# Optimization experiments

Hardware: AMD Instinct MI355X
Metric: run time of the kernel (lower is better)

Reference implementation:

```python
import jax, jax.numpy as jnp
import numpy as np

N_LETTERS = 256
EMBED_DIM = 1024
HIDDEN_DIM = 2048
SEQ_LEN = 4096


def setup_inputs() -> dict:
    key = jax.random.key(0)
    ks = jax.random.split(key, 8)
    s_e = 1.0 / np.sqrt(EMBED_DIM)
    s_h = 1.0 / np.sqrt(HIDDEN_DIM)
    return {
        "input_ids": jax.random.randint(ks[0], (SEQ_LEN,), 0, N_LETTERS, dtype=jnp.int64)
        if jax.config.jax_enable_x64 else jax.random.randint(ks[0], (SEQ_LEN,), 0, N_LETTERS, dtype=jnp.int32),
        "h0": jnp.zeros((1, 1, HIDDEN_DIM), jnp.float32),
        "c0": jnp.zeros((1, 1, HIDDEN_DIM), jnp.float32),
        "W_emb": jax.random.normal(ks[1], (N_LETTERS, EMBED_DIM), jnp.float32),
        "W_ih": jax.random.normal(ks[2], (4 * HIDDEN_DIM, EMBED_DIM), jnp.float32) * s_e,
        "W_hh": jax.random.normal(ks[3], (4 * HIDDEN_DIM, HIDDEN_DIM), jnp.float32) * s_h,
        "b_ih": jnp.zeros((4 * HIDDEN_DIM,), jnp.float32),
        "b_hh": jnp.zeros((4 * HIDDEN_DIM,), jnp.float32),
        "W_out": jax.random.normal(ks[4], (N_LETTERS, HIDDEN_DIM), jnp.float32) * s_h,
        "b_out": jnp.zeros((N_LETTERS,), jnp.float32),
    }


def reference(input_ids, h0, c0, W_emb, W_ih, W_hh, b_ih, b_hh, W_out, b_out):
    H = W_hh.shape[1]
    emb = W_emb[input_ids]                       # [L, E]
    # Precompute the input-side gate projections for all timesteps (batched GEMM).
    x_gates = emb @ W_ih.T + (b_ih + b_hh)       # [L, 4H]

    def step(carry, xg):
        h, c = carry                             # [H], [H]
        gates = xg + W_hh @ h                    # [4H], PyTorch order i,f,g,o
        i = jax.nn.sigmoid(gates[0 * H:1 * H])
        f = jax.nn.sigmoid(gates[1 * H:2 * H])
        g = jnp.tanh(gates[2 * H:3 * H])
        o = jax.nn.sigmoid(gates[3 * H:4 * H])
        c_new = f * c + i * g
        h_new = o * jnp.tanh(c_new)
        return (h_new, c_new), h_new

    (hL, cL), hs = jax.lax.scan(step, (h0[0, 0], c0[0, 0]), x_gates)  # hs: [L, H]
    logits = hs @ W_out.T + b_out                # [L, n_letters]
    # Dropout(p=0.1) is identity in eval mode.
    out = jax.nn.log_softmax(jax.nn.relu(logits), axis=-1)
    return out, hL[None, None, :], cL[None, None, :]
```

## Files before the change

### kernel.cpp

```cpp
#include <hip/hip_runtime.h>
#include <hip/hip_bf16.h>

#define SEQ 4096
#define EMB 1024
#define HID 2048
#define G4  8192
#define NL  256

typedef __attribute__((ext_vector_type(8))) short bf16x8;
typedef __attribute__((ext_vector_type(4))) float f32x4;

static __device__ __forceinline__ unsigned short f2bf(float f) {
    unsigned int x = __builtin_bit_cast(unsigned int, f);
    return (unsigned short)((x + 0x7FFFu + ((x >> 16) & 1u)) >> 16);
}
static __device__ __forceinline__ float bf2f(unsigned short u) {
    return __builtin_bit_cast(float, ((unsigned int)u) << 16);
}
static __device__ __forceinline__ unsigned long long aload(const unsigned long long* p) {
    return __hip_atomic_load(p, __ATOMIC_RELAXED, __HIP_MEMORY_SCOPE_AGENT);
}
static __device__ __forceinline__ float frcp(float x) {
    return __builtin_amdgcn_rcpf(x);
}
static __device__ __forceinline__ float fsigm(float x) {
    return frcp(1.f + __expf(-x));
}
static __device__ __forceinline__ float ftanh(float x) {
    return 1.f - 2.f * frcp(__expf(2.f * x) + 1.f);
}

__global__ __launch_bounds__(256) void k_f2b(const float* __restrict__ in,
                                             unsigned short* __restrict__ out, int n) {
    int i = (blockIdx.x * 256 + threadIdx.x) * 4;
    if (i < n) {
        float4 v = *(const float4*)&in[i];
        ushort4 u;
        u.x = f2bf(v.x); u.y = f2bf(v.y); u.z = f2bf(v.z); u.w = f2bf(v.w);
        *(ushort4*)&out[i] = u;
    }
}

__global__ __launch_bounds__(256) void k_emb(const int* __restrict__ ids,
                                             const float* __restrict__ W_emb,
                                             unsigned short* __restrict__ out) {
    int t = blockIdx.x;
    int e0 = threadIdx.x * 4;
    const float4 v = *(const float4*)&W_emb[(size_t)ids[t] * EMB + e0];
    ushort4 u;
    u.x = f2bf(v.x); u.y = f2bf(v.y); u.z = f2bf(v.z); u.w = f2bf(v.w);
    *(ushort4*)&out[(size_t)t * EMB + e0] = u;
}

#define BM 128
#define BN 128
#define BK 32
__global__ __launch_bounds__(256) void k_gemm_bt(
    const unsigned short* __restrict__ A, const unsigned short* __restrict__ B,
    const float* __restrict__ bias1, const float* __restrict__ bias2,
    float* __restrict__ Cf, unsigned short* __restrict__ Cb,
    int M, int N, int K)
{
    __shared__ unsigned short As[BM * BK];
    __shared__ unsigned short Bs[BN * BK];
    const int bm = blockIdx.x * BM;
    const int bn = blockIdx.y * BN;
    const int tid = threadIdx.x;
    const int wave = tid >> 6, lane = tid & 63;
    const int wm = (wave & 1) * 64, wn = (wave >> 1) * 64;
    const int row16 = lane & 15, quad = lane >> 4;

    f32x4 acc[4][4];
#pragma unroll
    for (int i = 0; i < 4; ++i)
#pragma unroll
        for (int j = 0; j < 4; ++j) acc[i][j] = (f32x4){0.f, 0.f, 0.f, 0.f};

    for (int k0 = 0; k0 < K; k0 += BK) {
        __syncthreads();
#pragma unroll
        for (int s = 0; s < 2; ++s) {
            int c = tid + s * 256;
            int r = c >> 2, col = (c & 3) * 8;
            *(uint4*)&As[r * BK + col] = *(const uint4*)&A[(size_t)(bm + r) * K + k0 + col];
            *(uint4*)&Bs[r * BK + col] = *(const uint4*)&B[(size_t)(bn + r) * K + k0 + col];
        }
        __syncthreads();
        bf16x8 af[4], bfr[4];
#pragma unroll
        for (int i = 0; i < 4; ++i) {
            af[i]  = *(const bf16x8*)&As[(wm + i * 16 + row16) * BK + quad * 8];
            bfr[i] = *(const bf16x8*)&Bs[(wn + i * 16 + row16) * BK + quad * 8];
        }
#pragma unroll
        for (int i = 0; i < 4; ++i)
#pragma unroll
            for (int j = 0; j < 4; ++j)
                acc[i][j] = __builtin_amdgcn_mfma_f32_16x16x32_bf16(af[i], bfr[j], acc[i][j], 0, 0, 0);
    }

#pragma unroll
    for (int j = 0; j < 4; ++j) {
        int col = bn + wn + j * 16 + row16;
        float bsum = (bias1 ? bias1[col] : 0.f) + (bias2 ? bias2[col] : 0.f);
#pragma unroll
        for (int i = 0; i < 4; ++i) {
#pragma unroll
            for (int r = 0; r < 4; ++r) {
                int row = bm + wm + i * 16 + quad * 4 + r;
                float v = acc[i][j][r] + bsum;
                if (Cf) Cf[(size_t)row * N + col] = v;
                else    Cb[(size_t)row * N + ((col & 2047) << 2) + (col >> 11)] = f2bf(v);
            }
        }
    }
}

#define LSTM_LDS 90112
__global__ __launch_bounds__(1024, 1) void k_lstm(
    const unsigned short* __restrict__ Whhb,
    const unsigned short* __restrict__ xg,
    const float* __restrict__ h0, const float* __restrict__ c0,
    unsigned short* __restrict__ hsb,
    float* __restrict__ outHC,
    unsigned long long* __restrict__ hcomm)
{
    extern __shared__ char smem[];
    float* LDSp = (float*)smem;

    const int b = blockIdx.x, tid = threadIdx.x;
    const int wave = tid >> 6, lane = tid & 63;
    const int sub = lane & 15, quad = lane >> 4;

    const int qa = (sub >> 3), qb = 2 + (sub >> 3), j = sub & 7;
    const unsigned short* wa = Whhb + ((size_t)(qa * HID + b * 8 + j)) * HID + wave * 128 + quad * 8;
    const unsigned short* wb = Whhb + ((size_t)(qb * HID + b * 8 + j)) * HID + wave * 128 + quad * 8;
    bf16x8 afrA[4], afrB[4];
#pragma unroll
    for (int c = 0; c < 4; ++c) {
        afrA[c] = *(const bf16x8*)(wa + c * 32);
        afrB[c] = *(const bf16x8*)(wb + c * 32);
    }

    float creg = 0.f;
    if (tid < 8) creg = c0[b * 8 + tid];

    for (int t = 0; t < SEQ; ++t) {
        float xq0 = 0.f, xq1 = 0.f, xq2 = 0.f, xq3 = 0.f;
        if (wave == 0 && lane < 8) {
            uint2 w2 = *(const uint2*)(xg + (size_t)t * G4 + (size_t)(b * 8 + lane) * 4);
            xq0 = bf2f((unsigned short)(w2.x & 0xffff));
            xq1 = bf2f((unsigned short)(w2.x >> 16));
            xq2 = bf2f((unsigned short)(w2.y & 0xffff));
            xq3 = bf2f((unsigned short)(w2.y >> 16));
        }

        f32x4 accA0 = (f32x4){0.f, 0.f, 0.f, 0.f};
        f32x4 accA1 = (f32x4){0.f, 0.f, 0.f, 0.f};
        f32x4 accB0 = (f32x4){0.f, 0.f, 0.f, 0.f};
        f32x4 accB1 = (f32x4){0.f, 0.f, 0.f, 0.f};

        if (t == 0) {
#pragma unroll
            for (int c = 0; c < 4; ++c) {
                const float* hp = h0 + wave * 128 + c * 32 + quad * 8;
                float4 va = *(const float4*)hp;
                float4 vb = *(const float4*)(hp + 4);
                uint4 d;
                d.x = (unsigned)f2bf(va.x) | ((unsigned)f2bf(va.y) << 16);
                d.y = (unsigned)f2bf(va.z) | ((unsigned)f2bf(va.w) << 16);
                d.z = (unsigned)f2bf(vb.x) | ((unsigned)f2bf(vb.y) << 16);
                d.w = (unsigned)f2bf(vb.z) | ((unsigned)f2bf(vb.w) << 16);
                bf16x8 hf = __builtin_bit_cast(bf16x8, d);
                if (c < 2) {
                    accA0 = __builtin_amdgcn_mfma_f32_16x16x32_bf16(afrA[c], hf, accA0, 0, 0, 0);
                    accB0 = __builtin_amdgcn_mfma_f32_16x16x32_bf16(afrB[c], hf, accB0, 0, 0, 0);
                } else {
                    accA1 = __builtin_amdgcn_mfma_f32_16x16x32_bf16(afrA[c], hf, accA1, 0, 0, 0);
                    accB1 = __builtin_amdgcn_mfma_f32_16x16x32_bf16(afrB[c], hf, accB1, 0, 0, 0);
                }
            }
        } else {
            const unsigned long long* sp =
                hcomm + (size_t)((t - 1) & 1) * 16384 + (size_t)(b & 7) * 2048
                      + (size_t)(wave * 16 + (lane >> 2)) * 8 + (lane & 3);
            const unsigned tag = (unsigned)t;
            unsigned long long x = aload(sp);
            if ((unsigned)(x >> 32) != tag) {
                __builtin_amdgcn_s_sleep(8);
                for (;;) {
                    unsigned long long x1 = aload(sp);
                    unsigned long long x2 = aload(sp);
                    if ((unsigned)(x1 >> 32) == tag) { x = x1; break; }
                    if ((unsigned)(x2 >> 32) == tag) { x = x2; break; }
                    __builtin_amdgcn_s_sleep(1);
                }
            }
            int myd = (int)(unsigned)x;
#pragma unroll
            for (int c = 0; c < 4; ++c) {
                const int sl = c * 16 + quad * 4;
                uint4 d;
                d.x = (unsigned)__shfl(myd, sl + 0);
                d.y = (unsigned)__shfl(myd, sl + 1);
                d.z = (unsigned)__shfl(myd, sl + 2);
                d.w = (unsigned)__shfl(myd, sl + 3);
                bf16x8 hf = __builtin_bit_cast(bf16x8, d);
                if (c < 2) {
                    accA0 = __builtin_amdgcn_mfma_f32_16x16x32_bf16(afrA[c], hf, accA0, 0, 0, 0);
                    accB0 = __builtin_amdgcn_mfma_f32_16x16x32_bf16(afrB[c], hf, accB0, 0, 0, 0);
                } else {
                    accA1 = __builtin_amdgcn_mfma_f32_16x16x32_bf16(afrA[c], hf, accA1, 0, 0, 0);
                    accB1 = __builtin_amdgcn_mfma_f32_16x16x32_bf16(afrB[c], hf, accB1, 0, 0, 0);
                }
            }
        }
        f32x4 acc0 = accA0 + accA1;
        f32x4 acc1 = accB0 + accB1;

        float* P = LDSp + (t & 1) * 640;
        if (sub == 0) {
#pragma unroll
            for (int r = 0; r < 4; ++r) {
                P[(quad * 4 + r) * 20 + wave]      = acc0[r];
                P[(16 + quad * 4 + r) * 20 + wave] = acc1[r];
            }
        }
        __syncthreads();

        if (wave == 0) {
            __builtin_amdgcn_s_setprio(1);
            float g = 0.f;
            if (lane < 32) {
                const float* rp = P + lane * 20;
                f32x4 s = *(const f32x4*)rp;
                s += *(const f32x4*)(rp + 4);
                s += *(const f32x4*)(rp + 8);
                s += *(const f32x4*)(rp + 12);
                g = s[0] + s[1] + s[2] + s[3];
            }
            float gF = __shfl(g, 8 + lane);
            float gG = __shfl(g, 16 + lane);
            float gO = __shfl(g, 24 + lane);
            unsigned hv = 0;
            float cn = 0.f, hn = 0.f;
            if (lane < 8) {
                float gi = g  + xq0;
                float gf = gF + xq1;
                float gg = gG + xq2;
                float go = gO + xq3;
                float i_ = fsigm(gi);
                float f_ = fsigm(gf);
                float g_ = ftanh(gg);
                float o_ = fsigm(go);
                cn = f_ * creg + i_ * g_;
                hn = o_ * ftanh(cn);
                creg = cn;
                hv = (unsigned)f2bf(hn);
            }
            {
                int jj = lane & 3;
                unsigned lo = (unsigned)__shfl((int)hv, 2 * jj);
                unsigned hi = (unsigned)__shfl((int)hv, 2 * jj + 1);
                if (lane < 32) {
                    unsigned long long wrd =
                        (((unsigned long long)(unsigned)(t + 1)) << 32)
                        | (unsigned long long)(lo | (hi << 16));
                    __hip_atomic_store(
                        &hcomm[(size_t)(t & 1) * 16384 + (size_t)(lane >> 2) * 2048 + b * 8 + jj],
                        wrd, __ATOMIC_RELAXED, __HIP_MEMORY_SCOPE_AGENT);
                }
            }
            __builtin_amdgcn_s_setprio(0);
            if (lane < 8) {
                hsb[(size_t)t * HID + b * 8 + lane] = (unsigned short)hv;
                if (t == SEQ - 1) {
                    outHC[b * 8 + lane] = hn;
                    outHC[HID + b * 8 + lane] = cn;
                }
            }
        }
    }
}

__global__ __launch_bounds__(256) void k_softmax(const float* __restrict__ logits,
                                                 float* __restrict__ out) {
    int row = blockIdx.x * 4 + (threadIdx.x >> 6);
    int lane = threadIdx.x & 63;
    const float* Lr = logits + (size_t)row * NL;
    float4 v = *(const float4*)&Lr[lane * 4];
    v.x = fmaxf(v.x, 0.f); v.y = fmaxf(v.y, 0.f);
    v.z = fmaxf(v.z, 0.f); v.w = fmaxf(v.w, 0.f);
    float m = fmaxf(fmaxf(v.x, v.y), fmaxf(v.z, v.w));
#pragma unroll
    for (int off = 32; off > 0; off >>= 1) m = fmaxf(m, __shfl_xor(m, off));
    float e = __expf(v.x - m) + __expf(v.y - m) + __expf(v.z - m) + __expf(v.w - m);
#pragma unroll
    for (int off = 32; off > 0; off >>= 1) e += __shfl_xor(e, off);
    float ls = __logf(e) + m;
    float4 o;
    o.x = v.x - ls; o.y = v.y - ls; o.z = v.z - ls; o.w = v.w - ls;
    *(float4*)&out[(size_t)row * NL + lane * 4] = o;
}

extern "C" void kernel_launch(void* const* d_in, const int* in_sizes, int n_in,
                              void* d_out, int out_size, void* d_ws, size_t ws_size,
                              hipStream_t stream) {
    const int*   ids   = (const int*)d_in[0];
    const float* h0    = (const float*)d_in[1];
    const float* c0    = (const float*)d_in[2];
    const float* W_emb = (const float*)d_in[3];
    const float* W_ih  = (const float*)d_in[4];
    const float* W_hh  = (const float*)d_in[5];
    const float* b_ih  = (const float*)d_in[6];
    const float* b_hh  = (const float*)d_in[7];
    const float* W_out = (const float*)d_in[8];
    const float* b_out = (const float*)d_in[9];
    float* out = (float*)d_out;

    char* ws = (char*)d_ws;
    unsigned short* xg    = (unsigned short*)(ws);
    unsigned short* hsb   = (unsigned short*)(ws + 67108864);
    unsigned short* Wihb  = (unsigned short*)(ws + 83886080);
    unsigned short* embb  = (unsigned short*)(ws + 100663296);
    unsigned short* Woutb = (unsigned short*)(ws + 109051904);
    float*          logit = (float*)(ws + 110100480);
    unsigned short* Whhb  = (unsigned short*)(ws + 114294784);
    unsigned long long* hcomm = (unsigned long long*)(ws + 147849216);

    k_f2b<<<(G4 * EMB / 4 + 255) / 256, 256, 0, stream>>>(W_ih, Wihb, G4 * EMB);
    k_f2b<<<(NL * HID / 4 + 255) / 256, 256, 0, stream>>>(W_out, Woutb, NL * HID);
    k_f2b<<<(G4 * HID / 4 + 255) / 256, 256, 0, stream>>>(W_hh, Whhb, G4 * HID);
    k_emb<<<SEQ, 256, 0, stream>>>(ids, W_emb, embb);

    dim3 g1(SEQ / BM, G4 / BN);
    k_gemm_bt<<<g1, 256, 0, stream>>>(embb, Wihb, b_ih, b_hh, nullptr, xg, SEQ, G4, EMB);

    hipFuncSetAttribute((const void*)k_lstm, hipFuncAttributeMaxDynamicSharedMemorySize, LSTM_LDS);
    k_lstm<<<256, 1024, LSTM_LDS, stream>>>(Whhb, xg, h0, c0, hsb, out + (size_t)SEQ * NL, hcomm);

    dim3 g2(SEQ / BM, NL / BN);
    k_gemm_bt<<<g2, 256, 0, stream>>>(hsb, Woutb, b_out, nullptr, logit, nullptr, SEQ, NL, HID);

    k_softmax<<<SEQ / 4, 256, 0, stream>>>(logit, out);
}
```

Measured before the change: 9.659 ms.

## Spread LSTM gate reduction and cell update across four waves

The per-step LDS reduction of the 16 wave partials and the gate nonlinearities, previously done serially by wave 0, are now split across four waves. Each wave handles two hidden units, using 64 lanes with a butterfly shuffle reduction. Each wave publishes its own packed h word to the cross-block communication buffer. The aim is to shorten the serial critical path of each recurrent step. The cost is more waves taking part in the tail of every step and more store instructions issued to hcomm.

Result: slower. 13.23 ms (+37.0%).

```diff
diff --git a/kernel.cpp b/kernel.cpp
--- a/kernel.cpp
+++ b/kernel.cpp
@@ -143,12 +143,13 @@
     }
 
     float creg = 0.f;
-    if (tid < 8) creg = c0[b * 8 + tid];
+    if (wave < 4 && (lane & 55) == 0) creg = c0[b * 8 + wave * 2 + (lane >> 3)];
 
     for (int t = 0; t < SEQ; ++t) {
         float xq0 = 0.f, xq1 = 0.f, xq2 = 0.f, xq3 = 0.f;
-        if (wave == 0 && lane < 8) {
-            uint2 w2 = *(const uint2*)(xg + (size_t)t * G4 + (size_t)(b * 8 + lane) * 4);
+        if (wave < 4 && (lane & 55) == 0) {
+            int u2 = b * 8 + wave * 2 + (lane >> 3);
+            uint2 w2 = *(const uint2*)(xg + (size_t)t * G4 + (size_t)u2 * 4);
             xq0 = bf2f((unsigned short)(w2.x & 0xffff));
             xq1 = bf2f((unsigned short)(w2.x >> 16));
             xq2 = bf2f((unsigned short)(w2.y & 0xffff));
@@ -228,55 +229,48 @@
         }
         __syncthreads();
 
-        if (wave == 0) {
+        if (wave < 4) {
             __builtin_amdgcn_s_setprio(1);
-            float g = 0.f;
-            if (lane < 32) {
-                const float* rp = P + lane * 20;
-                f32x4 s = *(const f32x4*)rp;
-                s += *(const f32x4*)(rp + 4);
-                s += *(const f32x4*)(rp + 8);
-                s += *(const f32x4*)(rp + 12);
-                g = s[0] + s[1] + s[2] + s[3];
-            }
-            float gF = __shfl(g, 8 + lane);
-            float gG = __shfl(g, 16 + lane);
-            float gO = __shfl(g, 24 + lane);
+            const int g = lane >> 4, e = (lane >> 3) & 1, part = lane & 7;
+            const float* rp = P + (g * 8 + wave * 2 + e) * 20 + part * 2;
+            float v = rp[0] + rp[1];
+            v += __shfl_xor(v, 1);
+            v += __shfl_xor(v, 2);
+            v += __shfl_xor(v, 4);
+            float gF = __shfl(v, (lane & 8) + 16);
+            float gG = __shfl(v, (lane & 8) + 32);
+            float gO = __shfl(v, (lane & 8) + 48);
             unsigned hv = 0;
             float cn = 0.f, hn = 0.f;
-            if (lane < 8) {
-                float gi = g  + xq0;
-                float gf = gF + xq1;
-                float gg = gG + xq2;
-                float go = gO + xq3;
-                float i_ = fsigm(gi);
-                float f_ = fsigm(gf);
-                float g_ = ftanh(gg);
-                float o_ = fsigm(go);
+            if ((lane & 55) == 0) {
+                float i_ = fsigm(v  + xq0);
+                float f_ = fsigm(gF + xq1);
+                float g_ = ftanh(gG + xq2);
+                float o_ = fsigm(gO + xq3);
                 cn = f_ * creg + i_ * g_;
                 hn = o_ * ftanh(cn);
                 creg = cn;
                 hv = (unsigned)f2bf(hn);
             }
             {
-                int jj = lane & 3;
-                unsigned lo = (unsigned)__shfl((int)hv, 2 * jj);
-                unsigned hi = (unsigned)__shfl((int)hv, 2 * jj + 1);
-                if (lane < 32) {
+                unsigned wlo = (unsigned)__shfl((int)hv, 0);
+                unsigned whi = (unsigned)__shfl((int)hv, 8);
+                if (lane < 8) {
                     unsigned long long wrd =
                         (((unsigned long long)(unsigned)(t + 1)) << 32)
-                        | (unsigned long long)(lo | (hi << 16));
+                        | (unsigned long long)(wlo | (whi << 16));
                     __hip_atomic_store(
-                        &hcomm[(size_t)(t & 1) * 16384 + (size_t)(lane >> 2) * 2048 + b * 8 + jj],
+                        &hcomm[(size_t)(t & 1) * 16384 + (size_t)lane * 2048 + b * 8 + wave],
                         wrd, __ATOMIC_RELAXED, __HIP_MEMORY_SCOPE_AGENT);
                 }
             }
             __builtin_amdgcn_s_setprio(0);
-            if (lane < 8) {
-                hsb[(size_t)t * HID + b * 8 + lane] = (unsigned short)hv;
+            if ((lane & 55) == 0) {
+                int u2 = b * 8 + wave * 2 + (lane >> 3);
+                hsb[(size_t)t * HID + u2] = (unsigned short)hv;
                 if (t == SEQ - 1) {
-                    outHC[b * 8 + lane] = hn;
-                    outHC[HID + b * 8 + lane] = cn;
+                    outHC[u2] = hn;
+                    outHC[HID + u2] = cn;
                 }
             }
         }
```
